# Kernel tuning notes

Measured on AMD Instinct MI355X. Metric: run time of the kernel, lower is better.

## Reference

```python
import jax, jax.numpy as jnp
import numpy as np

N_NODES = 100000
N_EDGES = 3200000
IN_DIM = 512
OUT_DIM = 128


def setup_inputs() -> dict:
    key = jax.random.key(0)
    kx, kw, kr, kc, kv = jax.random.split(key, 5)
    x = jax.random.normal(kx, (N_NODES, IN_DIM), dtype=jnp.float32)
    # glorot uniform init for the weight, matching glorot_init in the source
    init_range = np.sqrt(6.0 / (IN_DIM + OUT_DIM)).astype(np.float32)
    W = jax.random.uniform(kw, (IN_DIM, OUT_DIM), dtype=jnp.float32,
                           minval=-init_range, maxval=init_range)
    edge_row = jax.random.randint(kr, (N_EDGES,), 0, N_NODES, dtype=jnp.int32)
    edge_col = jax.random.randint(kc, (N_EDGES,), 0, N_NODES, dtype=jnp.int32)
    edge_val = jax.random.uniform(kv, (N_EDGES,), dtype=jnp.float32)
    return {"x": x, "W": W, "edge_row": edge_row, "edge_col": edge_col,
            "edge_val": edge_val}


def reference(x, W, edge_row, edge_col, edge_val):
    # dense projection: [N, in] @ [in, out] -> [N, out]
    xp = x @ W
    # SpMM: out[r] += val * xp[c] for each edge (r, c, val)
    msgs = xp[edge_col] * edge_val[:, None]          # [E, out]
    agg = jax.ops.segment_sum(msgs, edge_row, num_segments=N_NODES)
    return jax.nn.relu(agg)
```

## Files before the change

kernel.cpp:

```cpp
#include <hip/hip_runtime.h>

#define M_NODES 100000
#define MPAD    100096
#define K_DIM   512
#define N_DIM   128
#define NUM_EDGES 3200000

#define RSHIFT  6
#define ROWS_PB 64
#define NBUCK   1563
#define BCAP    2432
#define EPW     4096
#define NAPPEND ((NUM_EDGES + EPW - 1) / EPW)
#define GEMM_BLOCKS (MPAD / 128)

typedef __bf16 bf16x8 __attribute__((ext_vector_type(8)));
typedef float f32x16 __attribute__((ext_vector_type(16)));
typedef unsigned short ushort8 __attribute__((ext_vector_type(8)));
typedef unsigned short ushort4v __attribute__((ext_vector_type(4)));
typedef unsigned int uint32;

__device__ __forceinline__ unsigned short f2bf(float f) {
  uint32 u = __float_as_uint(f);
  u = (u + 0x7FFFu + ((u >> 16) & 1u)) >> 16;
  return (unsigned short)u;
}

__device__ __forceinline__ float bf_lo(uint32 m) {
  return __uint_as_float(m << 16);
}
__device__ __forceinline__ float bf_hi(uint32 m) {
  return __uint_as_float(m & 0xFFFF0000u);
}

__global__ __launch_bounds__(256) void wfrag_kernel(
    const float* __restrict__ W, unsigned short* __restrict__ Wf,
    int* __restrict__ gcursor) {
  const int t = blockIdx.x * 256 + threadIdx.x;
  const int j = t & 7;
  const int lane = (t >> 3) & 63;
  const int ng = (t >> 9) & 3;
  const int ks = t >> 11;
  const int k = ks * 16 + ((lane >> 5) << 3) + j;
  const int n = (ng << 5) + (lane & 31);
  Wf[t] = f2bf(W[k * N_DIM + n]);
  if (t < NBUCK) gcursor[t] = 0;
}

__device__ __forceinline__ void gemm_body(int bx, char* smem,
                                          const float* __restrict__ x,
                                          const unsigned short* __restrict__ Wf,
                                          unsigned short* __restrict__ xp) {
  auto As = (unsigned short(*)[72])smem;

  const int tid = threadIdx.x;
  const int w = tid >> 6;
  const int lane = tid & 63;
  const int l31 = lane & 31;
  const int lhi = lane >> 5;
  const int row0 = bx * 128;

  f32x16 acc[4] = {};
  float4 rg[8];

  auto load_tile = [&](int k0) {
#pragma unroll
    for (int it = 0; it < 8; ++it) {
      const int fidx = it * 256 + tid;
      const int rr = fidx >> 4;
      const int kq = fidx & 15;
      int gr = row0 + rr;
      if (gr >= M_NODES) gr = M_NODES - 1;
      rg[it] = *(const float4*)(x + (size_t)gr * K_DIM + k0 + kq * 4);
    }
  };

  load_tile(0);
  for (int k0 = 0; k0 < K_DIM; k0 += 64) {
#pragma unroll
    for (int it = 0; it < 8; ++it) {
      const int fidx = it * 256 + tid;
      const int rr = fidx >> 4;
      const int kq = fidx & 15;
      ushort4v b = {f2bf(rg[it].x), f2bf(rg[it].y), f2bf(rg[it].z),
                    f2bf(rg[it].w)};
      *(ushort4v*)(&As[rr][kq * 4]) = b;
    }
    __syncthreads();

    if (k0 + 64 < K_DIM) load_tile(k0 + 64);

    const int ksg0 = k0 >> 4;
#pragma unroll
    for (int ks = 0; ks < 4; ++ks) {
      const bf16x8 a = __builtin_bit_cast(
          bf16x8, *(const ushort8*)(&As[w * 32 + l31][ks * 16 + lhi * 8]));
      const ushort8* bp =
          (const ushort8*)(Wf) + ((size_t)(ksg0 + ks) * 4 * 64 + lane);
#pragma unroll
      for (int ng = 0; ng < 4; ++ng) {
        const bf16x8 b = __builtin_bit_cast(bf16x8, bp[(size_t)ng * 64]);
        acc[ng] =
            __builtin_amdgcn_mfma_f32_32x32x16_bf16(a, b, acc[ng], 0, 0, 0);
      }
    }
    __syncthreads();
  }

  const int rbase = row0 + w * 32 + 4 * lhi;
#pragma unroll
  for (int ng = 0; ng < 4; ++ng) {
    const int cc = (ng << 5) + l31;
#pragma unroll
    for (int reg = 0; reg < 16; ++reg) {
      const int rr = rbase + (reg & 3) + 8 * (reg >> 2);
      xp[(size_t)rr * N_DIM + cc] = f2bf(acc[ng][reg]);
    }
  }
}

__device__ __forceinline__ int tag_edge(int r, int* lcnt) {
  const int b = r >> RSHIFT;
  const int s = atomicAdd(&lcnt[b], 1);
  return (b << 18) | (s << 6) | (r & (ROWS_PB - 1));
}

__device__ __forceinline__ void emit_edge(int p, int col, float v,
                                          const int* lbase,
                                          uint2* __restrict__ buckets) {
  const int b = (int)((unsigned)p >> 18);
  const int idx = lbase[b] + ((p >> 6) & 0xFFF);
  if (idx < BCAP)
    buckets[(size_t)b * BCAP + idx] = make_uint2(
        ((uint32)col << 6) | (uint32)(p & (ROWS_PB - 1)), __float_as_uint(v));
}

__device__ __forceinline__ void bin_body(int bx, char* smem,
                                         const int* __restrict__ erow,
                                         const int* __restrict__ ecol,
                                         const float* __restrict__ eval,
                                         int* __restrict__ gcursor,
                                         uint2* __restrict__ buckets) {
  int* lcnt = (int*)smem;
  int* lbase = (int*)(smem + 6912);
  const int tid = threadIdx.x;
  for (int i = tid; i < NBUCK; i += 256) lcnt[i] = 0;
  __syncthreads();

  const int base = bx * EPW;
  int pk[16];
#pragma unroll
  for (int c = 0; c < 4; ++c) {
    const int e0 = base + c * 1024 + tid * 4;
    if (e0 < NUM_EDGES) {
      const int4 r4 = *(const int4*)(erow + e0);
      pk[c * 4 + 0] = tag_edge(r4.x, lcnt);
      pk[c * 4 + 1] = tag_edge(r4.y, lcnt);
      pk[c * 4 + 2] = tag_edge(r4.z, lcnt);
      pk[c * 4 + 3] = tag_edge(r4.w, lcnt);
    }
  }
  __syncthreads();

  for (int i = tid; i < NBUCK; i += 256) {
    const int c = lcnt[i];
    lbase[i] = c ? atomicAdd(&gcursor[i], c) : 0;
  }
  __syncthreads();

#pragma unroll
  for (int c = 0; c < 4; ++c) {
    const int e0 = base + c * 1024 + tid * 4;
    if (e0 < NUM_EDGES) {
      const int4 c4 = *(const int4*)(ecol + e0);
      const float4 v4 = *(const float4*)(eval + e0);
      emit_edge(pk[c * 4 + 0], c4.x, v4.x, lbase, buckets);
      emit_edge(pk[c * 4 + 1], c4.y, v4.y, lbase, buckets);
      emit_edge(pk[c * 4 + 2], c4.z, v4.z, lbase, buckets);
      emit_edge(pk[c * 4 + 3], c4.w, v4.w, lbase, buckets);
    }
  }
}

__global__ __launch_bounds__(256) void gemm_bin_kernel(
    const float* __restrict__ x, const unsigned short* __restrict__ Wf,
    unsigned short* __restrict__ xp, const int* __restrict__ erow,
    const int* __restrict__ ecol, const float* __restrict__ eval,
    int* __restrict__ gcursor, uint2* __restrict__ buckets) {
  __shared__ __align__(16) char smem[18432];
  if (blockIdx.x < GEMM_BLOCKS) {
    gemm_body(blockIdx.x, smem, x, Wf, xp);
  } else {
    bin_body(blockIdx.x - GEMM_BLOCKS, smem, erow, ecol, eval, gcursor,
             buckets);
  }
}

__global__ __launch_bounds__(256, 8) void bucket_gather_kernel(
    const unsigned short* __restrict__ xp, const int* __restrict__ gcursor,
    const uint2* __restrict__ buckets, float* __restrict__ out) {
  __shared__ uint2 eds[BCAP];
  __shared__ int rbase[ROWS_PB + 1];
  __shared__ int rcur[ROWS_PB];
  __shared__ int stmp[ROWS_PB];

  const int b = blockIdx.x;
  const int tid = threadIdx.x;
  int n = gcursor[b];
  if (n > BCAP) n = BCAP;

  if (tid < ROWS_PB) rcur[tid] = 0;
  __syncthreads();

  const uint2* bk = buckets + (size_t)b * BCAP;
  for (int i = tid; i < n; i += 256) atomicAdd(&rcur[bk[i].x & 63], 1);
  __syncthreads();

  if (tid < ROWS_PB) stmp[tid] = rcur[tid];
  __syncthreads();
  for (int off = 1; off < ROWS_PB; off <<= 1) {
    int v = 0, a = 0;
    if (tid < ROWS_PB) {
      v = stmp[tid];
      if (tid >= off) a = stmp[tid - off];
    }
    __syncthreads();
    if (tid < ROWS_PB) stmp[tid] = v + a;
    __syncthreads();
  }
  if (tid < ROWS_PB) {
    rbase[tid + 1] = stmp[tid];
    rcur[tid] = 0;
  }
  if (tid == 0) rbase[0] = 0;
  __syncthreads();

  for (int i = tid; i < n; i += 256) {
    const uint2 e = bk[i];
    const int rl = e.x & 63;
    const int pos = rbase[rl] + atomicAdd(&rcur[rl], 1);
    eds[pos] = e;
  }
  __syncthreads();

  const int wv = tid >> 6;
  const int lane = tid & 63;
  const uint32* xpl = (const uint32*)xp + lane;

  for (int rl = wv; rl < ROWS_PB; rl += 4) {
    const int row = (b << RSHIFT) + rl;
    if (row >= M_NODES) break;
    const int s = rbase[rl];
    const int e = rbase[rl + 1];

    float ax0 = 0.f, ay0 = 0.f, ax1 = 0.f, ay1 = 0.f;
    float ax2 = 0.f, ay2 = 0.f, ax3 = 0.f, ay3 = 0.f;
    int i = s;
    for (; i + 3 < e; i += 4) {
      const uint2 e0 = eds[i];
      const uint2 e1 = eds[i + 1];
      const uint2 e2 = eds[i + 2];
      const uint2 e3 = eds[i + 3];
      const uint32 m0 = xpl[(size_t)(e0.x >> 6) * 64];
      const uint32 m1 = xpl[(size_t)(e1.x >> 6) * 64];
      const uint32 m2 = xpl[(size_t)(e2.x >> 6) * 64];
      const uint32 m3 = xpl[(size_t)(e3.x >> 6) * 64];
      const float v0 = __uint_as_float(e0.y);
      const float v1 = __uint_as_float(e1.y);
      const float v2 = __uint_as_float(e2.y);
      const float v3 = __uint_as_float(e3.y);
      ax0 += v0 * bf_lo(m0); ay0 += v0 * bf_hi(m0);
      ax1 += v1 * bf_lo(m1); ay1 += v1 * bf_hi(m1);
      ax2 += v2 * bf_lo(m2); ay2 += v2 * bf_hi(m2);
      ax3 += v3 * bf_lo(m3); ay3 += v3 * bf_hi(m3);
    }
    for (; i < e; ++i) {
      const uint2 e0 = eds[i];
      const uint32 m0 = xpl[(size_t)(e0.x >> 6) * 64];
      const float v0 = __uint_as_float(e0.y);
      ax0 += v0 * bf_lo(m0);
      ay0 += v0 * bf_hi(m0);
    }

    float2 r;
    r.x = fmaxf((ax0 + ax1) + (ax2 + ax3), 0.f);
    r.y = fmaxf((ay0 + ay1) + (ay2 + ay3), 0.f);
    *(float2*)(out + (size_t)row * N_DIM + lane * 2) = r;
  }
}

extern "C" void kernel_launch(void* const* d_in, const int* in_sizes, int n_in,
                              void* d_out, int out_size, void* d_ws,
                              size_t ws_size, hipStream_t stream) {
  const float* x = (const float*)d_in[0];
  const float* W = (const float*)d_in[1];
  const int* erow = (const int*)d_in[2];
  const int* ecol = (const int*)d_in[3];
  const float* eval = (const float*)d_in[4];
  float* out = (float*)d_out;

  char* wsb = (char*)d_ws;
  size_t off = 0;
  auto alloc = [&](size_t bytes) {
    char* p = wsb + off;
    off = (off + bytes + 511) & ~(size_t)511;
    return p;
  };
  unsigned short* xp =
      (unsigned short*)alloc((size_t)MPAD * N_DIM * sizeof(unsigned short));
  unsigned short* Wf =
      (unsigned short*)alloc((size_t)K_DIM * N_DIM * sizeof(unsigned short));
  int* gcursor = (int*)alloc((size_t)NBUCK * sizeof(int));
  uint2* buckets = (uint2*)alloc((size_t)NBUCK * BCAP * sizeof(uint2));
  (void)ws_size;

  wfrag_kernel<<<(K_DIM * N_DIM) / 256, 256, 0, stream>>>(W, Wf, gcursor);

  gemm_bin_kernel<<<GEMM_BLOCKS + NAPPEND, 256, 0, stream>>>(
      x, Wf, xp, erow, ecol, eval, gcursor, buckets);

  bucket_gather_kernel<<<NBUCK, 256, 0, stream>>>(xp, gcursor, buckets, out);
}
```

Before: 498.1 us.

## Stage fp32 x tiles via direct global-to-LDS loads with double buffering

Replaces the register-staged load / bf16-convert / LDS-store path with __builtin_amdgcn_global_load_lds copies of raw fp32 tiles into swizzled, double-buffered shared memory. K-step drops to 32 and the bf16 conversion moves to fragment-read time. The aim is to cut register pressure and the extra VGPR-to-LDS store pass while overlapping the next tile's load with MFMA work. The trade-off is doubled LDS (32KB), which may lower occupancy for the fused bin blocks, plus repeated conversion work per read.

```diff
diff --git a/kernel.cpp b/kernel.cpp
--- a/kernel.cpp
+++ b/kernel.cpp
@@ -14,11 +14,16 @@
 #define NAPPEND ((NUM_EDGES + EPW - 1) / EPW)
 #define GEMM_BLOCKS (MPAD / 128)
 
+#define BK      32
+#define KSTEPS  (K_DIM / BK)
+
 typedef __bf16 bf16x8 __attribute__((ext_vector_type(8)));
 typedef float f32x16 __attribute__((ext_vector_type(16)));
 typedef unsigned short ushort8 __attribute__((ext_vector_type(8)));
-typedef unsigned short ushort4v __attribute__((ext_vector_type(4)));
 typedef unsigned int uint32;
+
+typedef __attribute__((address_space(1))) const unsigned int gas_u32;
+typedef __attribute__((address_space(3))) unsigned int las_u32;
 
 __device__ __forceinline__ unsigned short f2bf(float f) {
   uint32 u = __float_as_uint(f);
@@ -47,11 +52,42 @@
   if (t < NBUCK) gcursor[t] = 0;
 }
 
+__device__ __forceinline__ void stage_tile(float* dst,
+                                           const float* __restrict__ x,
+                                           int row0, int k0, int w, int lane) {
+#pragma unroll
+  for (int i = 0; i < 4; ++i) {
+    const int seg = i * 4 + w;
+    const int d = seg * 1024 + lane * 16;
+    const int row = d >> 7;
+    const int ch = (d >> 4) & 7;
+    const int sch = ch ^ (row & 7);
+    int gr = row0 + row;
+    if (gr >= M_NODES) gr = M_NODES - 1;
+    const float* src = x + (size_t)gr * K_DIM + k0 + sch * 4;
+    __builtin_amdgcn_global_load_lds((gas_u32*)src,
+                                     (las_u32*)(dst + seg * 256), 16, 0, 0);
+  }
+}
+
+__device__ __forceinline__ bf16x8 read_a_frag(const float* As, int r, int ks,
+                                              int hi) {
+  const int c0 = ks * 4 + hi * 2;
+  const int sw = r & 7;
+  const float4 f0 = *(const float4*)(As + r * 32 + ((c0 ^ sw) << 2));
+  const float4 f1 = *(const float4*)(As + r * 32 + (((c0 + 1) ^ sw) << 2));
+  ushort8 u;
+  u[0] = f2bf(f0.x); u[1] = f2bf(f0.y); u[2] = f2bf(f0.z); u[3] = f2bf(f0.w);
+  u[4] = f2bf(f1.x); u[5] = f2bf(f1.y); u[6] = f2bf(f1.z); u[7] = f2bf(f1.w);
+  return __builtin_bit_cast(bf16x8, u);
+}
+
 __device__ __forceinline__ void gemm_body(int bx, char* smem,
                                           const float* __restrict__ x,
                                           const unsigned short* __restrict__ Wf,
                                           unsigned short* __restrict__ xp) {
-  auto As = (unsigned short(*)[72])smem;
+  float* A0 = (float*)smem;
+  float* A1 = (float*)(smem + 16384);
 
   const int tid = threadIdx.x;
   const int w = tid >> 6;
@@ -59,42 +95,22 @@
   const int l31 = lane & 31;
   const int lhi = lane >> 5;
   const int row0 = bx * 128;
+  const int r = w * 32 + l31;
 
   f32x16 acc[4] = {};
-  float4 rg[8];
-
-  auto load_tile = [&](int k0) {
-#pragma unroll
-    for (int it = 0; it < 8; ++it) {
-      const int fidx = it * 256 + tid;
-      const int rr = fidx >> 4;
-      const int kq = fidx & 15;
-      int gr = row0 + rr;
-      if (gr >= M_NODES) gr = M_NODES - 1;
-      rg[it] = *(const float4*)(x + (size_t)gr * K_DIM + k0 + kq * 4);
-    }
-  };
-
-  load_tile(0);
-  for (int k0 = 0; k0 < K_DIM; k0 += 64) {
-#pragma unroll
-    for (int it = 0; it < 8; ++it) {
-      const int fidx = it * 256 + tid;
-      const int rr = fidx >> 4;
-      const int kq = fidx & 15;
-      ushort4v b = {f2bf(rg[it].x), f2bf(rg[it].y), f2bf(rg[it].z),
-                    f2bf(rg[it].w)};
-      *(ushort4v*)(&As[rr][kq * 4]) = b;
-    }
-    __syncthreads();
-
-    if (k0 + 64 < K_DIM) load_tile(k0 + 64);
-
-    const int ksg0 = k0 >> 4;
-#pragma unroll
-    for (int ks = 0; ks < 4; ++ks) {
-      const bf16x8 a = __builtin_bit_cast(
-          bf16x8, *(const ushort8*)(&As[w * 32 + l31][ks * 16 + lhi * 8]));
+
+  stage_tile(A0, x, row0, 0, w, lane);
+  __syncthreads();
+
+  for (int t = 0; t < KSTEPS; ++t) {
+    float* cur = (t & 1) ? A1 : A0;
+    float* nxt = (t & 1) ? A0 : A1;
+    if (t + 1 < KSTEPS) stage_tile(nxt, x, row0, (t + 1) * BK, w, lane);
+
+    const int ksg0 = t * 2;
+#pragma unroll
+    for (int ks = 0; ks < 2; ++ks) {
+      const bf16x8 a = read_a_frag(cur, r, ks, lhi);
       const ushort8* bp =
           (const ushort8*)(Wf) + ((size_t)(ksg0 + ks) * 4 * 64 + lane);
 #pragma unroll
@@ -187,7 +203,7 @@
     unsigned short* __restrict__ xp, const int* __restrict__ erow,
     const int* __restrict__ ecol, const float* __restrict__ eval,
     int* __restrict__ gcursor, uint2* __restrict__ buckets) {
-  __shared__ __align__(16) char smem[18432];
+  __shared__ __align__(16) char smem[32768];
   if (blockIdx.x < GEMM_BLOCKS) {
     gemm_body(blockIdx.x, smem, x, Wf, xp);
   } else {
```

After: 487.7 us. 2.1% less time.
